# Kernel tuning notes

Hardware: AMD Instinct MI355X
Metric: run time of the kernel (lower is better)

## Reference

```python
import jax, jax.numpy as jnp
import numpy as np

TEMPERATURE = 0.5
EPS = 1e-8  # torch CosineSimilarity eps


def setup_inputs() -> dict:
    key = jax.random.key(0)
    # x holds 2*batch_size concatenated embeddings (two augmented views)
    x = jax.random.normal(key, (4096, 512), dtype=jnp.float32)
    return {"x": x}


def reference(x) -> jnp.ndarray:
    n2 = x.shape[0]          # 2N rows
    n = n2 // 2
    # cosine similarity: normalize rows (clamped norm as in torch), then GEMM
    norms = jnp.maximum(jnp.linalg.norm(x, axis=1, keepdims=True), EPS)
    xn = x / norms
    sim = jnp.einsum('id,jd->ij', xn, xn) / TEMPERATURE  # [2N, 2N]
    # positive logit for row i is sim[i, (i+N) mod 2N]
    idx = jnp.arange(n2)
    pos = sim[idx, (idx + n) % n2]
    # CE with label 0 over logits = [pos, negatives]; since the logit set for
    # row i is exactly {sim[i, j] : j != i}, CE_i = logsumexp_{j!=i} sim[i,j] - pos_i
    sim_masked = jnp.where(jnp.eye(n2, dtype=bool), -jnp.inf, sim)
    lse = jax.nn.logsumexp(sim_masked, axis=1)
    # criterion uses reduction='sum' then divides by bsz -> mean
    return jnp.mean(lse - pos)
```

## Files before the change

### kernel.cpp

```cpp
#include <hip/hip_runtime.h>
#include <hip/hip_bf16.h>
#include <math.h>

typedef __bf16 bf16_t;
typedef __bf16 bf16x8 __attribute__((ext_vector_type(8)));
typedef float f32x4 __attribute__((ext_vector_type(4)));

#define N2 4096
#define NHALF 2048
#define DIM 512
#define TEMP_INV 2.0f

__global__ __launch_bounds__(256) void k_prep(const float* __restrict__ x,
                                              bf16_t* __restrict__ xn,
                                              float* __restrict__ rowsum) {
    const int pair = blockIdx.x * 4 + (threadIdx.x >> 6);
    const int lane = threadIdx.x & 63;
    const int rowi = pair;
    const int rowp = pair + NHALF;

    const float4* xi = reinterpret_cast<const float4*>(x + (size_t)rowi * DIM);
    const float4* xp = reinterpret_cast<const float4*>(x + (size_t)rowp * DIM);
    float4 a0 = xi[lane * 2], a1 = xi[lane * 2 + 1];
    float4 b0 = xp[lane * 2], b1 = xp[lane * 2 + 1];

    float ssi = a0.x*a0.x + a0.y*a0.y + a0.z*a0.z + a0.w*a0.w
              + a1.x*a1.x + a1.y*a1.y + a1.z*a1.z + a1.w*a1.w;
    float ssp = b0.x*b0.x + b0.y*b0.y + b0.z*b0.z + b0.w*b0.w
              + b1.x*b1.x + b1.y*b1.y + b1.z*b1.z + b1.w*b1.w;
#pragma unroll
    for (int off = 32; off; off >>= 1) {
        ssi += __shfl_xor(ssi, off, 64);
        ssp += __shfl_xor(ssp, off, 64);
    }
    const float sci = 1.0f / fmaxf(sqrtf(ssi), 1e-8f);
    const float scp = 1.0f / fmaxf(sqrtf(ssp), 1e-8f);

    float va[8] = {a0.x, a0.y, a0.z, a0.w, a1.x, a1.y, a1.z, a1.w};
    float vb[8] = {b0.x, b0.y, b0.z, b0.w, b1.x, b1.y, b1.z, b1.w};
    bf16x8 oi, op;
#pragma unroll
    for (int t = 0; t < 8; ++t) {
        oi[t] = (bf16_t)(va[t] * sci);
        op[t] = (bf16_t)(vb[t] * scp);
    }
    *reinterpret_cast<bf16x8*>(xn + (size_t)rowi * DIM + lane * 8) = oi;
    *reinterpret_cast<bf16x8*>(xn + (size_t)rowp * DIM + lane * 8) = op;

    if (threadIdx.x < 8) rowsum[blockIdx.x * 8 + threadIdx.x] = 0.0f;
}

__device__ __forceinline__ void load_lds16(const bf16_t* g, bf16_t* l) {
    __builtin_amdgcn_global_load_lds(
        (const __attribute__((address_space(1))) unsigned int*)g,
        (__attribute__((address_space(3))) unsigned int*)l,
        16, 0, 0);
}

__global__ __launch_bounds__(256) void k_simgemm(const bf16_t* __restrict__ xn,
                                                 float* __restrict__ rowsum,
                                                 float* __restrict__ pos) {
    __shared__ bf16_t As[3][128 * 32];
    __shared__ bf16_t Bs[3][128 * 32];
    __shared__ float  rpA[128];
    __shared__ float  rpB[128];

    const int t = blockIdx.x;
    int bn = (int)((sqrtf(8.0f * (float)t + 1.0f) - 1.0f) * 0.5f);
    while ((bn * (bn + 1)) / 2 > t) --bn;
    while (((bn + 1) * (bn + 2)) / 2 <= t) ++bn;
    const int bm = t - (bn * (bn + 1)) / 2;
    const bool diagb = (bm == bn);

    const int tid  = threadIdx.x;
    const int lane = tid & 63;
    const int wid  = tid >> 6;
    const int wr   = wid >> 1;
    const int wc   = wid & 1;
    const int q    = lane >> 4;
    const int l15  = lane & 15;

    if (tid < 128) { rpA[tid] = 0.0f; rpB[tid] = 0.0f; }

    const int slot_g = (tid & 3) ^ ((tid >> 3) & 3);
    const bf16_t* gA = xn + (size_t)(bm * 128 + (tid >> 2)) * DIM + slot_g * 8;
    const bf16_t* gB = xn + (size_t)(bn * 128 + (tid >> 2)) * DIM + slot_g * 8;

    const int rsw = (q ^ ((l15 >> 1) & 3)) * 8;
    const int arow = (wr * 64 + l15) * 32 + rsw;
    const int brow = (wc * 64 + l15) * 32 + rsw;

    f32x4 acc[4][4] = {};

    load_lds16(gA,                         &As[0][tid * 8]);
    load_lds16(gA + (size_t)64 * DIM,      &As[0][2048 + tid * 8]);
    load_lds16(gB,                         &Bs[0][tid * 8]);
    load_lds16(gB + (size_t)64 * DIM,      &Bs[0][2048 + tid * 8]);
    load_lds16(gA + 32,                    &As[1][tid * 8]);
    load_lds16(gA + (size_t)64 * DIM + 32, &As[1][2048 + tid * 8]);
    load_lds16(gB + 32,                    &Bs[1][tid * 8]);
    load_lds16(gB + (size_t)64 * DIM + 32, &Bs[1][2048 + tid * 8]);

#pragma unroll
    for (int kt = 0; kt < 16; ++kt) {
        if (kt < 15) asm volatile("s_waitcnt vmcnt(4)" ::: "memory");
        else         asm volatile("s_waitcnt vmcnt(0)" ::: "memory");
        __builtin_amdgcn_s_barrier();
        __builtin_amdgcn_sched_barrier(0);

        if (kt + 2 < 16) {
            const int nb = (kt + 2) % 3;
            const bf16_t* gA2 = gA + (kt + 2) * 32;
            const bf16_t* gB2 = gB + (kt + 2) * 32;
            load_lds16(gA2,                    &As[nb][tid * 8]);
            load_lds16(gA2 + (size_t)64 * DIM, &As[nb][2048 + tid * 8]);
            load_lds16(gB2,                    &Bs[nb][tid * 8]);
            load_lds16(gB2 + (size_t)64 * DIM, &Bs[nb][2048 + tid * 8]);
        }

        const int cb = kt % 3;
        bf16x8 af[4], bv[4];
#pragma unroll
        for (int mt = 0; mt < 4; ++mt)
            af[mt] = *reinterpret_cast<const bf16x8*>(&As[cb][arow + mt * 512]);
#pragma unroll
        for (int nt = 0; nt < 4; ++nt)
            bv[nt] = *reinterpret_cast<const bf16x8*>(&Bs[cb][brow + nt * 512]);
#pragma unroll
        for (int mt = 0; mt < 4; ++mt)
#pragma unroll
            for (int nt = 0; nt < 4; ++nt)
                acc[mt][nt] = __builtin_amdgcn_mfma_f32_16x16x32_bf16(
                    af[mt], bv[nt], acc[mt][nt], 0, 0, 0);
    }

    const bool dmask = diagb && (wr == wc);
    const bool pmask = (bn == bm + 16) && (wr == wc);
    float colacc[4] = {0.0f, 0.0f, 0.0f, 0.0f};
#pragma unroll
    for (int mt = 0; mt < 4; ++mt) {
        float rowp[4] = {0.0f, 0.0f, 0.0f, 0.0f};
#pragma unroll
        for (int nt = 0; nt < 4; ++nt)
#pragma unroll
            for (int r = 0; r < 4; ++r) {
                float e = __expf(TEMP_INV * acc[mt][nt][r]);
                if (mt == nt) {
                    const bool hit = (l15 == q * 4 + r);
                    if (dmask && hit) e = 0.0f;
                    if (pmask && hit) {
                        const float pv = TEMP_INV * acc[mt][nt][r];
                        const int gr = bm * 128 + wr * 64 + mt * 16 + q * 4 + r;
                        pos[gr] = pv;
                        pos[gr + NHALF] = pv;
                    }
                }
                rowp[r] += e;
                colacc[nt] += e;
            }
#pragma unroll
        for (int r = 0; r < 4; ++r) {
            float p = rowp[r];
            p += __shfl_xor(p, 1, 64);
            p += __shfl_xor(p, 2, 64);
            p += __shfl_xor(p, 4, 64);
            p += __shfl_xor(p, 8, 64);
            if (l15 == 0) atomicAdd(&rpA[wr * 64 + mt * 16 + q * 4 + r], p);
        }
    }
    if (!diagb) {
#pragma unroll
        for (int nt = 0; nt < 4; ++nt) {
            float c = colacc[nt];
            c += __shfl_xor(c, 16, 64);
            c += __shfl_xor(c, 32, 64);
            if (q == 0) atomicAdd(&rpB[wc * 64 + nt * 16 + l15], c);
        }
    }
    __syncthreads();
    if (tid < 128) {
        atomicAdd(&rowsum[bm * 128 + tid], rpA[tid]);
    } else if (!diagb) {
        atomicAdd(&rowsum[bn * 128 + (tid - 128)], rpB[tid - 128]);
    }
}

__global__ __launch_bounds__(256) void k_finalize(const float* __restrict__ rowsum,
                                                  const float* __restrict__ pos,
                                                  float* __restrict__ out) {
    __shared__ float red[256];
    const float4* rs4 = reinterpret_cast<const float4*>(rowsum);
    const float4* ps4 = reinterpret_cast<const float4*>(pos);
    float s = 0.0f;
#pragma unroll
    for (int it = 0; it < 4; ++it) {
        const int i = it * 256 + threadIdx.x;
        float4 r = rs4[i];
        float4 p = ps4[i];
        s += __logf(r.x) - p.x;
        s += __logf(r.y) - p.y;
        s += __logf(r.z) - p.z;
        s += __logf(r.w) - p.w;
    }
    red[threadIdx.x] = s;
    __syncthreads();
    for (int st = 128; st; st >>= 1) {
        if (threadIdx.x < st) red[threadIdx.x] += red[threadIdx.x + st];
        __syncthreads();
    }
    if (threadIdx.x == 0) out[0] = red[0] / (float)N2;
}

extern "C" void kernel_launch(void* const* d_in, const int* in_sizes, int n_in,
                              void* d_out, int out_size, void* d_ws, size_t ws_size,
                              hipStream_t stream) {
    (void)in_sizes; (void)n_in; (void)out_size; (void)ws_size;
    const float* x = (const float*)d_in[0];
    float* out = (float*)d_out;

    char* ws = (char*)d_ws;
    bf16_t* xn     = (bf16_t*)ws;
    float*  rowsum = (float*)(ws + (size_t)N2 * DIM * 2);
    float*  pos    = rowsum + N2;

    k_prep<<<512, 256, 0, stream>>>(x, xn, rowsum);
    k_simgemm<<<528, 256, 0, stream>>>(xn, rowsum, pos);
    k_finalize<<<1, 256, 0, stream>>>(rowsum, pos, out);
}
```

Measured before the change: 85.10 us.

## Deepen LDS prefetch pipeline to four stages and remap block order across XCDs

Raises the shared-memory ring buffer from three to four stages so three K-tiles are in flight, adjusting the vmcnt waits to match. Also permutes the block index so consecutive triangular tiles go to the same XCD (blockIdx & 7 selects a contiguous chunk of 66 tiles), aiming to improve L2 reuse of the shared row panels. LDS use rises from about 48KB to 64KB per block, which may lower occupancy.

```diff
diff --git a/kernel.cpp b/kernel.cpp
--- a/kernel.cpp
+++ b/kernel.cpp
@@ -60,12 +60,12 @@
 __global__ __launch_bounds__(256) void k_simgemm(const bf16_t* __restrict__ xn,
                                                  float* __restrict__ rowsum,
                                                  float* __restrict__ pos) {
-    __shared__ bf16_t As[3][128 * 32];
-    __shared__ bf16_t Bs[3][128 * 32];
+    __shared__ bf16_t As[4][128 * 32];
+    __shared__ bf16_t Bs[4][128 * 32];
     __shared__ float  rpA[128];
     __shared__ float  rpB[128];
 
-    const int t = blockIdx.x;
+    const int t = (blockIdx.x & 7) * 66 + (blockIdx.x >> 3);
     int bn = (int)((sqrtf(8.0f * (float)t + 1.0f) - 1.0f) * 0.5f);
     while ((bn * (bn + 1)) / 2 > t) --bn;
     while (((bn + 1) * (bn + 2)) / 2 <= t) ++bn;
@@ -92,33 +92,33 @@
 
     f32x4 acc[4][4] = {};
 
-    load_lds16(gA,                         &As[0][tid * 8]);
-    load_lds16(gA + (size_t)64 * DIM,      &As[0][2048 + tid * 8]);
-    load_lds16(gB,                         &Bs[0][tid * 8]);
-    load_lds16(gB + (size_t)64 * DIM,      &Bs[0][2048 + tid * 8]);
-    load_lds16(gA + 32,                    &As[1][tid * 8]);
-    load_lds16(gA + (size_t)64 * DIM + 32, &As[1][2048 + tid * 8]);
-    load_lds16(gB + 32,                    &Bs[1][tid * 8]);
-    load_lds16(gB + (size_t)64 * DIM + 32, &Bs[1][2048 + tid * 8]);
+#pragma unroll
+    for (int p = 0; p < 3; ++p) {
+        load_lds16(gA + p * 32,                    &As[p][tid * 8]);
+        load_lds16(gA + (size_t)64 * DIM + p * 32, &As[p][2048 + tid * 8]);
+        load_lds16(gB + p * 32,                    &Bs[p][tid * 8]);
+        load_lds16(gB + (size_t)64 * DIM + p * 32, &Bs[p][2048 + tid * 8]);
+    }
 
 #pragma unroll
     for (int kt = 0; kt < 16; ++kt) {
-        if (kt < 15) asm volatile("s_waitcnt vmcnt(4)" ::: "memory");
-        else         asm volatile("s_waitcnt vmcnt(0)" ::: "memory");
+        if (kt < 14)       asm volatile("s_waitcnt vmcnt(8)" ::: "memory");
+        else if (kt == 14) asm volatile("s_waitcnt vmcnt(4)" ::: "memory");
+        else               asm volatile("s_waitcnt vmcnt(0)" ::: "memory");
         __builtin_amdgcn_s_barrier();
         __builtin_amdgcn_sched_barrier(0);
 
-        if (kt + 2 < 16) {
-            const int nb = (kt + 2) % 3;
-            const bf16_t* gA2 = gA + (kt + 2) * 32;
-            const bf16_t* gB2 = gB + (kt + 2) * 32;
-            load_lds16(gA2,                    &As[nb][tid * 8]);
-            load_lds16(gA2 + (size_t)64 * DIM, &As[nb][2048 + tid * 8]);
-            load_lds16(gB2,                    &Bs[nb][tid * 8]);
-            load_lds16(gB2 + (size_t)64 * DIM, &Bs[nb][2048 + tid * 8]);
+        if (kt + 3 < 16) {
+            const int nb = (kt + 3) & 3;
+            const bf16_t* gA3 = gA + (kt + 3) * 32;
+            const bf16_t* gB3 = gB + (kt + 3) * 32;
+            load_lds16(gA3,                    &As[nb][tid * 8]);
+            load_lds16(gA3 + (size_t)64 * DIM, &As[nb][2048 + tid * 8]);
+            load_lds16(gB3,                    &Bs[nb][tid * 8]);
+            load_lds16(gB3 + (size_t)64 * DIM, &Bs[nb][2048 + tid * 8]);
         }
 
-        const int cb = kt % 3;
+        const int cb = kt & 3;
         bf16x8 af[4], bv[4];
 #pragma unroll
         for (int mt = 0; mt < 4; ++mt)
```

Measured after the change: 85.48 us. No clear change (+0.4%).
